# Performance work log

Measured on AMD Instinct MI355X. Metric: run time of the kernel, lower is better.

The kernel has to match this reference:

```python
import jax, jax.numpy as jnp
import numpy as np

N_NODES = 100000
N_EDGES = 640000
H = 128

def setup_inputs() -> dict:
    key = jax.random.key(0)
    k = jax.random.split(key, 8)
    x_src = jax.random.normal(k[0], (N_NODES, H), dtype=jnp.float32)
    x_dst = jax.random.normal(k[1], (N_NODES, H), dtype=jnp.float32)
    src_idx = jax.random.randint(k[2], (N_EDGES,), 0, N_NODES, dtype=jnp.int64)
    dst_idx = jax.random.randint(k[3], (N_EDGES,), 0, N_NODES, dtype=jnp.int64)
    # torch Linear default init: U(-1/sqrt(fan_in), 1/sqrt(fan_in)); randn*scale is fine for a numeric baseline
    W1 = jax.random.normal(k[4], (H, 2 * H), dtype=jnp.float32) * (1.0 / np.sqrt(2 * H))
    b1 = jnp.zeros((H,), dtype=jnp.float32)
    W2 = jax.random.normal(k[5], (1, H), dtype=jnp.float32) * (1.0 / np.sqrt(H))
    b2 = jnp.zeros((1,), dtype=jnp.float32)
    return {"x_src": x_src, "x_dst": x_dst, "src_idx": src_idx, "dst_idx": dst_idx,
            "W1": W1, "b1": b1, "W2": W2, "b2": b2}

def reference(x_src, x_dst, src_idx, dst_idx, W1, b1, W2, b2):
    # per-edge gather of endpoint features, concat -> [E, 2H]
    h = jnp.concatenate([x_src[src_idx], x_dst[dst_idx]], axis=1)
    h = jax.nn.relu(h @ W1.T + b1)            # [E, H]
    score = (h @ W2.T + b2)[:, 0]             # [E]
    return score
```

## Files before the change

kernel.cpp:

```cpp
#include <hip/hip_runtime.h>
#include <hip/hip_bf16.h>

typedef __bf16 bf16x8 __attribute__((ext_vector_type(8)));
typedef __bf16 bf16x4 __attribute__((ext_vector_type(4)));
typedef float  f32x4  __attribute__((ext_vector_type(4)));

#define HF 128
#define W1K 256

__global__ __launch_bounds__(256) void w1_repack(
    const float* __restrict__ W1, __bf16* __restrict__ wf)
{
    const int h    = blockIdx.x;
    const int tid  = threadIdx.x;
    const int lane = tid & 63;
    const int wid  = tid >> 6;
    const int l15  = lane & 15;
    const int lg   = lane >> 4;

    for (int f = wid; f < 32; f += 4) {
        const int mt = f >> 2;
        const int kk = f & 3;
        const float* p = W1 + h * HF + (size_t)(mt * 16 + l15) * W1K
                       + kk * 32 + lg * 8;
        f32x4 a = *reinterpret_cast<const f32x4*>(p);
        f32x4 b = *reinterpret_cast<const f32x4*>(p + 4);
        bf16x8 w8;
        #pragma unroll
        for (int i = 0; i < 4; ++i) {
            w8[i]     = (__bf16)a[i];
            w8[i + 4] = (__bf16)b[i];
        }
        *reinterpret_cast<bf16x8*>(wf + ((size_t)(h * 32 + f) * 64 + lane) * 8) = w8;
    }
}

__global__ __launch_bounds__(512, 1) void node_precompute13(
    const float* __restrict__ x_src, const float* __restrict__ x_dst,
    const __bf16* __restrict__ wf,
    __bf16* __restrict__ u, __bf16* __restrict__ v, int nNodes)
{
    __shared__ __align__(16) float xlds[8][2][2048];

    const int tid  = threadIdx.x;
    const int lane = tid & 63;
    const int wid  = tid >> 6;
    const int l15  = lane & 15;
    const int lg   = lane >> 4;

    const int h = wid & 1;
    const float* __restrict__ xh = h ? x_dst : x_src;
    __bf16* __restrict__ oph = h ? v : u;

    bf16x8 wfrag[32];
    {
        const __bf16* wsrc = wf + ((size_t)h * 32 * 64 + lane) * 8;
        #pragma unroll
        for (int f = 0; f < 32; ++f)
            wfrag[f] = *reinterpret_cast<const bf16x8*>(wsrc + (size_t)f * 64 * 8);
    }

    const int nst    = nNodes >> 4;
    const int stride = gridDim.x * 4;

    auto STAGE = [&](int buf, int st) {
        #pragma unroll
        for (int i = 0; i < 8; ++i) {
            const int G   = i * 64 + lane;
            const int row = G >> 5;
            const int q   = G & 31;
            const int qs  = q ^ (row & 7);
            const int grow = min(st * 16 + row, nNodes - 1);
            const float* src = xh + (size_t)grow * HF + qs * 4;
            __builtin_amdgcn_global_load_lds(
                (const __attribute__((address_space(1))) void*)src,
                (__attribute__((address_space(3))) void*)&xlds[wid][buf][(size_t)G * 4],
                16, 0, 0);
        }
    };

    int st = blockIdx.x * 4 + (wid >> 1);
    if (st >= nst) return;
    STAGE(0, st);
    asm volatile("s_waitcnt vmcnt(0)" ::: "memory");
    __builtin_amdgcn_sched_barrier(0);

    int buf = 0;
    while (st < nst) {
        const int stn = st + stride;
        const bool more = (stn < nst);
        if (more) {
            STAGE(buf ^ 1, stn);
            asm volatile("s_waitcnt vmcnt(16)" ::: "memory");
        } else {
            asm volatile("s_waitcnt vmcnt(8)" ::: "memory");
        }
        __builtin_amdgcn_sched_barrier(0);

        f32x4 acc[8];
        #pragma unroll
        for (int mt = 0; mt < 8; ++mt) acc[mt] = (f32x4){0.f, 0.f, 0.f, 0.f};

        const float* xr = &xlds[wid][buf][(size_t)l15 * 128];
        #pragma unroll
        for (int kk = 0; kk < 4; ++kk) {
            const int q0 = kk * 8 + lg * 2;
            f32x4 a0 = *reinterpret_cast<const f32x4*>(xr + ((q0)     ^ (l15 & 7)) * 4);
            f32x4 a1 = *reinterpret_cast<const f32x4*>(xr + ((q0 + 1) ^ (l15 & 7)) * 4);
            bf16x8 xb;
            #pragma unroll
            for (int i = 0; i < 4; ++i) {
                xb[i]     = (__bf16)a0[i];
                xb[i + 4] = (__bf16)a1[i];
            }
            #pragma unroll
            for (int mt = 0; mt < 8; ++mt)
                acc[mt] = __builtin_amdgcn_mfma_f32_16x16x32_bf16(
                    wfrag[mt * 4 + kk], xb, acc[mt], 0, 0, 0);
        }

        {
            const int node = st * 16 + l15;
            __bf16* op = oph + (size_t)node * HF + lg * 4;
            #pragma unroll
            for (int mt = 0; mt < 8; ++mt) {
                bf16x4 o4;
                #pragma unroll
                for (int r = 0; r < 4; ++r) o4[r] = (__bf16)acc[mt][r];
                *reinterpret_cast<bf16x4*>(op + mt * 16) = o4;
            }
        }

        buf ^= 1;
        st = stn;
    }
}

__global__ __launch_bounds__(256) void edge_score_kernel(
    const __bf16* __restrict__ u, const __bf16* __restrict__ v,
    const int* __restrict__ sidx, const int* __restrict__ didx,
    const float* __restrict__ W2, const float* __restrict__ b1,
    const float* __restrict__ b2,
    float* __restrict__ out, int nEdges)
{
    const int tid = threadIdx.x;
    const int sub = tid >> 4;
    const int l16 = tid & 15;

    const int ebase = blockIdx.x * 128 + sub;

    float w2v[8], b1v[8];
    #pragma unroll
    for (int j = 0; j < 8; ++j) {
        w2v[j] = W2[l16 * 8 + j];
        b1v[j] = b1[l16 * 8 + j];
    }
    const float b2v = b2[0];

    int e[8], si[8], di[8];
    #pragma unroll
    for (int q = 0; q < 8; ++q) {
        e[q] = ebase + q * 16;
        const int c = min(e[q], nEdges - 1);
        si[q] = sidx[c];
        di[q] = didx[c];
    }

    bf16x8 uv[8], vv[8];
    #pragma unroll
    for (int q = 0; q < 8; ++q) {
        uv[q] = *reinterpret_cast<const bf16x8*>(u + (size_t)si[q] * HF + l16 * 8);
        vv[q] = *reinterpret_cast<const bf16x8*>(v + (size_t)di[q] * HF + l16 * 8);
    }

    float s[8];
    #pragma unroll
    for (int q = 0; q < 8; ++q) {
        float acc = 0.f;
        #pragma unroll
        for (int j = 0; j < 8; ++j)
            acc += fmaxf((float)uv[q][j] + (float)vv[q][j] + b1v[j], 0.f) * w2v[j];
        s[q] = acc;
    }

    #pragma unroll
    for (int off = 1; off < 16; off <<= 1)
        #pragma unroll
        for (int q = 0; q < 8; ++q)
            s[q] += __shfl_xor(s[q], off, 64);

    if (l16 == 0) {
        #pragma unroll
        for (int q = 0; q < 8; ++q)
            if (e[q] < nEdges) out[e[q]] = s[q] + b2v;
    }
}

__global__ __launch_bounds__(256, 2) void edge_mlp_kernel(
    const float* __restrict__ x_src, const float* __restrict__ x_dst,
    const int*   __restrict__ src_idx, const int* __restrict__ dst_idx,
    const float* __restrict__ W1, const float* __restrict__ b1,
    const float* __restrict__ W2, const float* __restrict__ b2,
    float* __restrict__ out, int nEdges)
{
    __shared__ __align__(16) __bf16 w1lds[64 * 64 * 8];

    const int tid  = threadIdx.x;
    const int lane = tid & 63;
    const int wid  = tid >> 6;
    const int l15  = lane & 15;
    const int lg   = lane >> 4;

    for (int p = wid; p < 64; p += 4) {
        const int n   = p >> 3;
        const int kk  = p & 7;
        const float* src = W1 + (n * 16 + l15) * W1K + kk * 32 + lg * 8;
        bf16x8 w8;
        #pragma unroll
        for (int i = 0; i < 8; ++i) w8[i] = (__bf16)src[i];
        *reinterpret_cast<bf16x8*>(&w1lds[(p * 64 + lane) * 8]) = w8;
    }
    __syncthreads();

    float w2v[8], b1v[8];
    #pragma unroll
    for (int n = 0; n < 8; ++n) {
        w2v[n] = W2[n * 16 + l15];
        b1v[n] = b1[n * 16 + l15];
    }
    const float b2v = b2[0];

    const int ntiles = nEdges / 256;
    for (int t = blockIdx.x; t < ntiles; t += gridDim.x) {
        const int ebase = t * 256 + wid * 64;

        const float* srow[4];
        const float* drow[4];
        #pragma unroll
        for (int m = 0; m < 4; ++m) {
            const int e  = ebase + m * 16 + l15;
            srow[m] = x_src + (size_t)src_idx[e] * HF + lg * 8;
            drow[m] = x_dst + (size_t)dst_idx[e] * HF + lg * 8;
        }

        f32x4 acc[4][8];
        #pragma unroll
        for (int m = 0; m < 4; ++m)
            #pragma unroll
            for (int n = 0; n < 8; ++n)
                acc[m][n] = (f32x4){0.f, 0.f, 0.f, 0.f};

        #pragma unroll
        for (int kk = 0; kk < 8; ++kk) {
            bf16x8 a[4];
            #pragma unroll
            for (int m = 0; m < 4; ++m) {
                const float* p = (kk < 4) ? (srow[m] + kk * 32)
                                          : (drow[m] + (kk - 4) * 32);
                f32x4 u0 = *reinterpret_cast<const f32x4*>(p);
                f32x4 u1 = *reinterpret_cast<const f32x4*>(p + 4);
                bf16x8 av;
                #pragma unroll
                for (int i = 0; i < 4; ++i) {
                    av[i]     = (__bf16)u0[i];
                    av[i + 4] = (__bf16)u1[i];
                }
                a[m] = av;
            }
            #pragma unroll
            for (int n = 0; n < 8; ++n) {
                bf16x8 bfrag = *reinterpret_cast<const bf16x8*>(
                    &w1lds[((n * 8 + kk) * 64 + lane) * 8]);
                #pragma unroll
                for (int m = 0; m < 4; ++m) {
                    acc[m][n] = __builtin_amdgcn_mfma_f32_16x16x32_bf16(
                        a[m], bfrag, acc[m][n], 0, 0, 0);
                }
            }
        }

        #pragma unroll
        for (int m = 0; m < 4; ++m) {
            float part[4];
            #pragma unroll
            for (int r = 0; r < 4; ++r) {
                float s = 0.f;
                #pragma unroll
                for (int n = 0; n < 8; ++n) {
                    float hv = acc[m][n][r] + b1v[n];
                    s += fmaxf(hv, 0.f) * w2v[n];
                }
                part[r] = s;
            }
            #pragma unroll
            for (int off = 1; off < 16; off <<= 1) {
                #pragma unroll
                for (int r = 0; r < 4; ++r)
                    part[r] += __shfl_xor(part[r], off, 64);
            }
            if (l15 == m) {
                f32x4 v4 = { part[0] + b2v, part[1] + b2v,
                             part[2] + b2v, part[3] + b2v };
                *reinterpret_cast<f32x4*>(&out[ebase + m * 16 + lg * 4]) = v4;
            }
        }
    }
}

extern "C" void kernel_launch(void* const* d_in, const int* in_sizes, int n_in,
                              void* d_out, int out_size, void* d_ws, size_t ws_size,
                              hipStream_t stream) {
    const float* x_src  = (const float*)d_in[0];
    const float* x_dst  = (const float*)d_in[1];
    const int*   sidx   = (const int*)d_in[2];
    const int*   didx   = (const int*)d_in[3];
    const float* W1     = (const float*)d_in[4];
    const float* b1     = (const float*)d_in[5];
    const float* W2     = (const float*)d_in[6];
    const float* b2     = (const float*)d_in[7];
    float* out = (float*)d_out;

    const int nEdges = in_sizes[2];
    const int nNodes = in_sizes[0] / HF;

    const size_t uvsz   = (size_t)2 * nNodes * HF;
    const size_t needed = uvsz * sizeof(__bf16) + 64 * 1024;
    if (ws_size >= needed && (nNodes & 15) == 0) {
        __bf16* u  = (__bf16*)d_ws;
        __bf16* v  = u + (size_t)nNodes * HF;
        __bf16* wf = u + uvsz;

        w1_repack<<<2, 256, 0, stream>>>(W1, wf);

        node_precompute13<<<256, 512, 0, stream>>>(
            x_src, x_dst, wf, u, v, nNodes);

        const int egrid = (nEdges + 127) / 128;
        edge_score_kernel<<<egrid, 256, 0, stream>>>(
            u, v, sidx, didx, W2, b1, b2, out, nEdges);
    } else {
        edge_mlp_kernel<<<512, 256, 0, stream>>>(
            x_src, x_dst, sidx, didx, W1, b1, W2, b2, out, nEdges);
    }
}
```

Measured before the change: 82.22 us.

## Triple-buffer node precompute with 8-row stages and halve edges per block

The node precompute kernel now stages 8 node rows per step instead of 16 and uses three LDS buffers, so two global loads are in flight while one is consumed, with vmcnt waits adjusted to match. Each 16x16 MFMA tile now carries only 8 valid nodes, which wastes half of the MFMA work and leaves half the lanes idle on stores. In exchange the loads get deeper prefetch. The edge score kernel handles 4 edges per thread group instead of 8 and launches twice as many blocks, trading per-thread memory-level parallelism for more parallel blocks.

Result: no change. 81.07 us (median of 2 runs) (-1.4%).

```diff
diff --git a/kernel.cpp b/kernel.cpp
--- a/kernel.cpp
+++ b/kernel.cpp
@@ -35,12 +35,12 @@
     }
 }
 
-__global__ __launch_bounds__(512, 1) void node_precompute13(
+__global__ __launch_bounds__(512, 1) void node_precompute14(
     const float* __restrict__ x_src, const float* __restrict__ x_dst,
     const __bf16* __restrict__ wf,
     __bf16* __restrict__ u, __bf16* __restrict__ v, int nNodes)
 {
-    __shared__ __align__(16) float xlds[8][2][2048];
+    __shared__ __align__(16) float xlds[8][3][1024];
 
     const int tid  = threadIdx.x;
     const int lane = tid & 63;
@@ -60,40 +60,50 @@
             wfrag[f] = *reinterpret_cast<const bf16x8*>(wsrc + (size_t)f * 64 * 8);
     }
 
-    const int nst    = nNodes >> 4;
+    const int nst    = nNodes >> 3;
     const int stride = gridDim.x * 4;
 
     auto STAGE = [&](int buf, int st) {
-        #pragma unroll
-        for (int i = 0; i < 8; ++i) {
+        float* dst0 = &xlds[wid][buf][0];
+        #pragma unroll
+        for (int i = 0; i < 4; ++i) {
             const int G   = i * 64 + lane;
             const int row = G >> 5;
             const int q   = G & 31;
-            const int qs  = q ^ (row & 7);
-            const int grow = min(st * 16 + row, nNodes - 1);
+            const int qs  = q ^ row;
+            const int grow = min(st * 8 + row, nNodes - 1);
             const float* src = xh + (size_t)grow * HF + qs * 4;
             __builtin_amdgcn_global_load_lds(
                 (const __attribute__((address_space(1))) void*)src,
-                (__attribute__((address_space(3))) void*)&xlds[wid][buf][(size_t)G * 4],
+                (__attribute__((address_space(3))) void*)(dst0 + (size_t)G * 4),
                 16, 0, 0);
         }
     };
 
     int st = blockIdx.x * 4 + (wid >> 1);
     if (st >= nst) return;
+
     STAGE(0, st);
-    asm volatile("s_waitcnt vmcnt(0)" ::: "memory");
-    __builtin_amdgcn_sched_barrier(0);
-
-    int buf = 0;
+    if (st + stride < nst) STAGE(1, st + stride);
+
+    int it = 0;
+    int bcur = 0;
+    const int row_l = l15 & 7;
     while (st < nst) {
-        const int stn = st + stride;
-        const bool more = (stn < nst);
-        if (more) {
-            STAGE(buf ^ 1, stn);
-            asm volatile("s_waitcnt vmcnt(16)" ::: "memory");
+        const int st1 = st + stride;
+        const int st2 = st + 2 * stride;
+        const bool hn = (st1 < nst);
+        const bool ha = (st2 < nst);
+        if (ha) STAGE((bcur + 2) % 3, st2);
+
+        if (it == 0) {
+            if (ha)      asm volatile("s_waitcnt vmcnt(8)"  ::: "memory");
+            else if (hn) asm volatile("s_waitcnt vmcnt(4)"  ::: "memory");
+            else         asm volatile("s_waitcnt vmcnt(0)"  ::: "memory");
         } else {
-            asm volatile("s_waitcnt vmcnt(8)" ::: "memory");
+            if (ha)      asm volatile("s_waitcnt vmcnt(16)" ::: "memory");
+            else if (hn) asm volatile("s_waitcnt vmcnt(12)" ::: "memory");
+            else         asm volatile("s_waitcnt vmcnt(8)"  ::: "memory");
         }
         __builtin_amdgcn_sched_barrier(0);
 
@@ -101,12 +111,12 @@
         #pragma unroll
         for (int mt = 0; mt < 8; ++mt) acc[mt] = (f32x4){0.f, 0.f, 0.f, 0.f};
 
-        const float* xr = &xlds[wid][buf][(size_t)l15 * 128];
+        const float* xr = &xlds[wid][bcur][(size_t)row_l * 128];
         #pragma unroll
         for (int kk = 0; kk < 4; ++kk) {
             const int q0 = kk * 8 + lg * 2;
-            f32x4 a0 = *reinterpret_cast<const f32x4*>(xr + ((q0)     ^ (l15 & 7)) * 4);
-            f32x4 a1 = *reinterpret_cast<const f32x4*>(xr + ((q0 + 1) ^ (l15 & 7)) * 4);
+            f32x4 a0 = *reinterpret_cast<const f32x4*>(xr + ((q0)     ^ row_l) * 4);
+            f32x4 a1 = *reinterpret_cast<const f32x4*>(xr + ((q0 + 1) ^ row_l) * 4);
             bf16x8 xb;
             #pragma unroll
             for (int i = 0; i < 4; ++i) {
@@ -119,8 +129,8 @@
                     wfrag[mt * 4 + kk], xb, acc[mt], 0, 0, 0);
         }
 
-        {
-            const int node = st * 16 + l15;
+        if (l15 < 8) {
+            const int node = st * 8 + l15;
             __bf16* op = oph + (size_t)node * HF + lg * 4;
             #pragma unroll
             for (int mt = 0; mt < 8; ++mt) {
@@ -131,8 +141,9 @@
             }
         }
 
-        buf ^= 1;
-        st = stn;
+        bcur = (bcur + 1) % 3;
+        st = st1;
+        ++it;
     }
 }
 
@@ -147,7 +158,7 @@
     const int sub = tid >> 4;
     const int l16 = tid & 15;
 
-    const int ebase = blockIdx.x * 128 + sub;
+    const int ebase = blockIdx.x * 64 + sub;
 
     float w2v[8], b1v[8];
     #pragma unroll
@@ -157,41 +168,38 @@
     }
     const float b2v = b2[0];
 
-    int e[8], si[8], di[8];
-    #pragma unroll
-    for (int q = 0; q < 8; ++q) {
+    int e[4], si[4], di[4];
+    #pragma unroll
+    for (int q = 0; q < 4; ++q) {
         e[q] = ebase + q * 16;
         const int c = min(e[q], nEdges - 1);
         si[q] = sidx[c];
         di[q] = didx[c];
     }
 
-    bf16x8 uv[8], vv[8];
-    #pragma unroll
-    for (int q = 0; q < 8; ++q) {
+    bf16x8 uv[4], vv[4];
+    #pragma unroll
+    for (int q = 0; q < 4; ++q) {
         uv[q] = *reinterpret_cast<const bf16x8*>(u + (size_t)si[q] * HF + l16 * 8);
         vv[q] = *reinterpret_cast<const bf16x8*>(v + (size_t)di[q] * HF + l16 * 8);
     }
 
-    float s[8];
-    #pragma unroll
-    for (int q = 0; q < 8; ++q) {
-        float acc = 0.f;
+    float s[4] = {0.f, 0.f, 0.f, 0.f};
+    #pragma unroll
+    for (int q = 0; q < 4; ++q)
         #pragma unroll
         for (int j = 0; j < 8; ++j)
-            acc += fmaxf((float)uv[q][j] + (float)vv[q][j] + b1v[j], 0.f) * w2v[j];
-        s[q] = acc;
-    }
+            s[q] += fmaxf((float)uv[q][j] + (float)vv[q][j] + b1v[j], 0.f) * w2v[j];
 
     #pragma unroll
     for (int off = 1; off < 16; off <<= 1)
         #pragma unroll
-        for (int q = 0; q < 8; ++q)
+        for (int q = 0; q < 4; ++q)
             s[q] += __shfl_xor(s[q], off, 64);
 
     if (l16 == 0) {
         #pragma unroll
-        for (int q = 0; q < 8; ++q)
+        for (int q = 0; q < 4; ++q)
             if (e[q] < nEdges) out[e[q]] = s[q] + b2v;
     }
 }
@@ -325,17 +333,17 @@
 
     const size_t uvsz   = (size_t)2 * nNodes * HF;
     const size_t needed = uvsz * sizeof(__bf16) + 64 * 1024;
-    if (ws_size >= needed && (nNodes & 15) == 0) {
+    if (ws_size >= needed && (nNodes & 7) == 0) {
         __bf16* u  = (__bf16*)d_ws;
         __bf16* v  = u + (size_t)nNodes * HF;
         __bf16* wf = u + uvsz;
 
         w1_repack<<<2, 256, 0, stream>>>(W1, wf);
 
-        node_precompute13<<<256, 512, 0, stream>>>(
+        node_precompute14<<<256, 512, 0, stream>>>(
             x_src, x_dst, wf, u, v, nNodes);
 
-        const int egrid = (nEdges + 127) / 128;
+        const int egrid = (nEdges + 63) / 64;
         edge_score_kernel<<<egrid, 256, 0, stream>>>(
             u, v, sidx, didx, W2, b1, b2, out, nEdges);
     } else {
```
